# Kernel tuning notes

Hardware: AMD Instinct MI355X
Metric: run time of the kernel (lower is better)

The kernel has to match this reference:

```python
import jax, jax.numpy as jnp
import numpy as np

D_MODEL = 1024
BASE = 7
NUM_PLANES = 2
EPS = 1e-6


def setup_inputs() -> dict:
    key = jax.random.key(0)
    k_x, k_w, k_t, k_g = jax.random.split(key, 4)
    B, S, D = 4, 8192, D_MODEL
    x = jax.random.normal(k_x, (B, S, D), dtype=jnp.float32)
    # eidosTransform params: linear 3D -> D, then 2 planes of learned rotation angles over D/2 pairs
    W = jax.random.normal(k_w, (3 * D, D), dtype=jnp.float32) / np.sqrt(3 * D)
    b = jnp.zeros((D,), dtype=jnp.float32)
    theta = jax.random.normal(k_t, (NUM_PLANES, D // 2), dtype=jnp.float32) * 0.1
    # ModularPhaseNorm gain
    gamma = jnp.ones((D,), dtype=jnp.float32)
    return {"x": x, "W": W, "b": b, "theta": theta, "gamma": gamma}


def _eidos_transform(t, W, b, theta):
    # linear projection 3D -> D ('truncate' collapse to d_out)
    y = jnp.einsum("bse,ed->bsd", t, W) + b  # [B,S,D]
    B, S, D = y.shape
    # geometric mode: rotate (even, odd) dim pairs by learned angles, per plane
    for p in range(NUM_PLANES):
        yp = y.reshape(B, S, D // 2, 2)
        a, c2 = yp[..., 0], yp[..., 1]
        cos_t = jnp.cos(theta[p])
        sin_t = jnp.sin(theta[p])
        ra = a * cos_t - c2 * sin_t
        rb = a * sin_t + c2 * cos_t
        y = jnp.stack([ra, rb], axis=-1).reshape(B, S, D)
    return y


def _modular_phase_norm(y, gamma):
    # RMS-normalize within feature groups defined by (dim index mod BASE)
    D = y.shape[-1]
    group = jnp.arange(D) % BASE                      # [D]
    onehot = jax.nn.one_hot(group, BASE, dtype=y.dtype)  # [D, BASE]
    counts = onehot.sum(axis=0)                       # [BASE]
    ss = jnp.einsum("bsd,dg->bsg", y * y, onehot)     # [B,S,BASE]
    rms = jnp.sqrt(ss / counts + EPS)                 # [B,S,BASE]
    denom = rms[..., group]                           # [B,S,D]
    return y / denom * gamma


def reference(x, W, b, theta, gamma):
    B, S, D = x.shape
    zero_row = jnp.zeros((B, 1, D), dtype=x.dtype)
    left = jnp.concatenate([zero_row, x[:, :-1, :]], axis=1)   # roll +1, zero first
    right = jnp.concatenate([x[:, 1:, :], zero_row], axis=1)   # roll -1, zero last
    triplet = jnp.concatenate([left, x, right], axis=-1)        # [B,S,3D]
    mixed = _eidos_transform(triplet, W, b, theta)
    return _modular_phase_norm(mixed, gamma)
```

## Files before the change

### kernel.cpp

```cpp
#include <hip/hip_runtime.h>
#include <hip/hip_bf16.h>
#include <stdint.h>


#define SEQ 8192
#define NB 4
#define DM 1024
#define KD 3072

typedef __attribute__((ext_vector_type(8))) short short8_t;
typedef __attribute__((ext_vector_type(4))) float f32x4;

__device__ __forceinline__ unsigned short f2bf(float f) {
  union { float f; uint32_t u; } v; v.f = f;
  return (unsigned short)((v.u + 0x7fffu + ((v.u >> 16) & 1u)) >> 16);
}

__device__ __forceinline__ void async_ld16(const void* g, void* l) {
  __builtin_amdgcn_global_load_lds(
      (const __attribute__((address_space(1))) uint32_t*)g,
      (__attribute__((address_space(3))) uint32_t*)(uint32_t)(uintptr_t)l,
      16, 0, 0);
}

__global__ __launch_bounds__(256) void prep_w(const float* __restrict__ W,
                                              const float* __restrict__ theta,
                                              unsigned short* __restrict__ Wt) {
  __shared__ float csc[32], css[32];
  __shared__ unsigned short tile[64][72];
  const int bk = blockIdx.x % 48, bn = blockIdx.x / 48;
  const int k0 = bk * 64, n0 = bn * 64;
  const int t = threadIdx.x;
  if (t < 32) {
    int d = n0 / 2 + t;
    float ang = theta[d] + theta[512 + d];
    csc[t] = cosf(ang); css[t] = sinf(ang);
  }
  __syncthreads();
#pragma unroll
  for (int i = 0; i < 8; ++i) {
    int idx = i * 256 + t;
    int pr = idx >> 5;
    int pc = idx & 31;
    const float2 w2 = *(const float2*)&W[(size_t)(k0 + pr) * DM + n0 + pc * 2];
    float c = csc[pc], s = css[pc];
    tile[pc * 2][pr]     = f2bf(w2.x * c - w2.y * s);
    tile[pc * 2 + 1][pr] = f2bf(w2.x * s + w2.y * c);
  }
  __syncthreads();
#pragma unroll
  for (int i = 0; i < 16; ++i) {
    int idx = i * 256 + t;
    int r = idx >> 6, cdx = idx & 63;
    Wt[(size_t)(n0 + r) * KD + k0 + cdx] = tile[r][cdx];
  }
}

__global__ void prep_bias(const float* __restrict__ b, const float* __restrict__ theta,
                          float* __restrict__ biasp, float* __restrict__ zp) {
  const int t = threadIdx.x;
  float ang = theta[t] + theta[512 + t];
  float c = cosf(ang), s = sinf(ang);
  float be = b[2 * t], bo = b[2 * t + 1];
  biasp[2 * t]     = be * c - bo * s;
  biasp[2 * t + 1] = be * s + bo * c;
  if (t < 256) ((float4*)zp)[t] = make_float4(0.f, 0.f, 0.f, 0.f);
}

__global__ __launch_bounds__(256) void prep_x(const float* __restrict__ x,
                                              unsigned short* __restrict__ xbp) {
  const size_t total = (size_t)NB * 8194 * 128;
  for (size_t i = (size_t)blockIdx.x * 256 + threadIdx.x; i < total;
       i += (size_t)gridDim.x * 256) {
    int d8 = (int)(i & 127);
    size_t rem = i >> 7;
    int sp = (int)(rem % 8194);
    size_t bb = rem / 8194;
    uint4 o = make_uint4(0u, 0u, 0u, 0u);
    if (sp > 0 && sp < 8193) {
      const float4* src = (const float4*)(x + (bb * SEQ + (size_t)(sp - 1)) * DM + d8 * 8);
      float4 lo = src[0], hi = src[1];
      o.x = (uint32_t)f2bf(lo.x) | ((uint32_t)f2bf(lo.y) << 16);
      o.y = (uint32_t)f2bf(lo.z) | ((uint32_t)f2bf(lo.w) << 16);
      o.z = (uint32_t)f2bf(hi.x) | ((uint32_t)f2bf(hi.y) << 16);
      o.w = (uint32_t)f2bf(hi.z) | ((uint32_t)f2bf(hi.w) << 16);
    }
    ((uint4*)xbp)[i] = o;
  }
}

__global__ __launch_bounds__(512, 2) void gemm256(const unsigned short* __restrict__ xbp,
                                                  const unsigned short* __restrict__ Wt,
                                                  const float* __restrict__ biasp,
                                                  float* __restrict__ out) {
  __shared__ __align__(16) unsigned char As[4][16384];
  __shared__ __align__(16) unsigned char Bs[4][16384];

  const int tid = threadIdx.x;
  const int lane = tid & 63;
  const int wid = tid >> 6;
  const int wm = wid >> 2, wn = wid & 3;
  const int row16 = lane & 15, kgrp = lane >> 4;

  const int L = blockIdx.x;
  const int xcd = L & 7;
  const int j = L >> 3;
  const int mtile = xcd * 16 + (j >> 2);
  const int ntile = j & 3;

  const int n0 = ntile * 256;
  const int batch = mtile >> 5;
  const int s0 = (mtile & 31) * 256;
  const size_t m0 = (size_t)mtile * 256;

  auto stageA = [&](int kt, int buf) {
    const int c = kt >> 5;
    const int ksb = (kt & 31) * 32;
    const size_t base = ((size_t)batch * 8194 + (size_t)(s0 + c)) * DM + ksb;
#pragma unroll
    for (int i = 0; i < 2; ++i) {
      int idx = i * 512 + tid;
      int row = idx >> 2, c16 = idx & 3;
      int cs = c16 ^ ((row >> 1) & 3);
      async_ld16(xbp + base + (size_t)row * DM + cs * 8, &As[buf][idx * 16]);
    }
  };
  auto stageB = [&](int kt, int buf) {
    const int kb = kt * 32;
#pragma unroll
    for (int i = 0; i < 2; ++i) {
      int idx = i * 512 + tid;
      int row = idx >> 2, c16 = idx & 3;
      int cs = c16 ^ ((row >> 1) & 3);
      async_ld16(Wt + (size_t)(n0 + row) * KD + kb + cs * 8, &Bs[buf][idx * 16]);
    }
  };

  f32x4 acc[8][4];
#pragma unroll
  for (int a = 0; a < 8; ++a)
#pragma unroll
    for (int b = 0; b < 4; ++b) acc[a][b] = (f32x4){0.f, 0.f, 0.f, 0.f};

  stageA(0, 0); stageB(0, 0);
  stageA(1, 1); stageB(1, 1);
  stageA(2, 2); stageB(2, 2);
  asm volatile("s_waitcnt vmcnt(8)" ::: "memory");
  __builtin_amdgcn_s_barrier();

  for (int kt = 0; kt < 96; ++kt) {
    const int buf = kt & 3, sbuf = (kt + 3) & 3;
    const unsigned char* Ab = As[buf];
    const unsigned char* Bb = Bs[buf];
    short8_t af[4], bf[4];

#pragma unroll
    for (int mi = 0; mi < 4; ++mi) {
      int r = wm * 128 + mi * 16 + row16;
      af[mi] = *(const short8_t*)(Ab + r * 64 + (kgrp ^ ((r >> 1) & 3)) * 16);
    }
#pragma unroll
    for (int ni = 0; ni < 4; ++ni) {
      int r = wn * 64 + ni * 16 + row16;
      bf[ni] = *(const short8_t*)(Bb + r * 64 + (kgrp ^ ((r >> 1) & 3)) * 16);
    }
    if (kt < 93) stageA(kt + 3, sbuf);
    __builtin_amdgcn_s_barrier();
    asm volatile("s_waitcnt lgkmcnt(0)" ::: "memory");
    __builtin_amdgcn_sched_barrier(0);
    __builtin_amdgcn_s_setprio(1);
#pragma unroll
    for (int mi = 0; mi < 4; ++mi)
#pragma unroll
      for (int ni = 0; ni < 4; ++ni)
        acc[mi][ni] = __builtin_amdgcn_mfma_f32_16x16x32_bf16(
            af[mi], bf[ni], acc[mi][ni], 0, 0, 0);
    __builtin_amdgcn_s_setprio(0);
    __builtin_amdgcn_s_barrier();

#pragma unroll
    for (int mi = 0; mi < 4; ++mi) {
      int r = wm * 128 + 64 + mi * 16 + row16;
      af[mi] = *(const short8_t*)(Ab + r * 64 + (kgrp ^ ((r >> 1) & 3)) * 16);
    }
    if (kt < 93) stageB(kt + 3, sbuf);
    __builtin_amdgcn_s_barrier();
    asm volatile("s_waitcnt lgkmcnt(0)" ::: "memory");
    __builtin_amdgcn_sched_barrier(0);
    __builtin_amdgcn_s_setprio(1);
#pragma unroll
    for (int mi = 0; mi < 4; ++mi)
#pragma unroll
      for (int ni = 0; ni < 4; ++ni)
        acc[mi + 4][ni] = __builtin_amdgcn_mfma_f32_16x16x32_bf16(
            af[mi], bf[ni], acc[mi + 4][ni], 0, 0, 0);
    __builtin_amdgcn_s_setprio(0);
    if (kt < 93)      asm volatile("s_waitcnt vmcnt(8)" ::: "memory");
    else if (kt == 93) asm volatile("s_waitcnt vmcnt(4)" ::: "memory");
    else if (kt == 94) asm volatile("s_waitcnt vmcnt(0)" ::: "memory");
    __builtin_amdgcn_s_barrier();
  }

#pragma unroll
  for (int mi = 0; mi < 8; ++mi) {
    size_t grow = m0 + (size_t)(wm * 128 + mi * 16 + kgrp * 4);
#pragma unroll
    for (int ni = 0; ni < 4; ++ni) {
      int col = n0 + wn * 64 + ni * 16 + row16;
      float bia = biasp[col];
      float* op = out + grow * DM + col;
#pragma unroll
      for (int r = 0; r < 4; ++r) op[(size_t)r * DM] = acc[mi][ni][r] + bia;
    }
  }
}

__global__ __launch_bounds__(256) void gemm_fb(const float* __restrict__ Ag,
                                               const unsigned short* __restrict__ Wt,
                                               const float* __restrict__ biasp,
                                               const float* __restrict__ zp,
                                               float* __restrict__ out) {
  __shared__ __align__(16) unsigned char As[128 * 64 * 4];
  __shared__ __align__(16) unsigned char Bs[128 * 64 * 2];

  const int tid = threadIdx.x;
  const int lane = tid & 63;
  const int wid = tid >> 6;
  const int wm = wid >> 1, wn = wid & 1;
  const int row16 = lane & 15, kgrp = lane >> 4;

  const int L = blockIdx.x;
  const int xcd = L & 7;
  const int j = L >> 3;
  const int mtile = xcd * 32 + (j >> 3);
  const int ntile = j & 7;

  const int n0 = ntile * 128;
  const int batch = mtile >> 6;
  const int s0 = (mtile & 63) * 128;
  const size_t m0 = (size_t)mtile * 128;

  f32x4 acc[4][4];
#pragma unroll
  for (int a = 0; a < 4; ++a)
#pragma unroll
    for (int b = 0; b < 4; ++b) acc[a][b] = (f32x4){0.f, 0.f, 0.f, 0.f};

  for (int kt = 0; kt < 48; ++kt) {
    const int c = kt >> 4;
    const int ksb = (kt & 15) * 64;
    __syncthreads();
#pragma unroll
    for (int it = 0; it < 8; ++it) {
      int f16 = it * 256 + tid;
      int row = f16 >> 4, c16 = f16 & 15;
      int c16s = c16 ^ (row & 7);
      int s = s0 + row + c - 1;
      const float* src = (s >= 0 && s < SEQ)
          ? Ag + ((size_t)batch * SEQ + (size_t)s) * DM + ksb + c16s * 4
          : zp + c16s * 4;
      async_ld16(src, As + f16 * 16);
    }
#pragma unroll
    for (int it = 0; it < 4; ++it) {
      int f16 = it * 256 + tid;
      int row = f16 >> 3, c16 = f16 & 7;
      int c16s = c16 ^ (row & 7);
      const unsigned short* src = Wt + (size_t)(n0 + row) * KD + kt * 64 + c16s * 8;
      async_ld16(src, Bs + f16 * 16);
    }
    __syncthreads();

#pragma unroll
    for (int kk = 0; kk < 2; ++kk) {
      short8_t af[4], bfr[4];
#pragma unroll
      for (int mi = 0; mi < 4; ++mi) {
        int r = wm * 64 + mi * 16 + row16;
        int kb = kk * 128 + kgrp * 32;
        f32x4 lo = *(const f32x4*)(As + r * 256 + (kb ^ ((r & 7) << 4)));
        f32x4 hi = *(const f32x4*)(As + r * 256 + ((kb + 16) ^ ((r & 7) << 4)));
        union { short8_t v; unsigned short u[8]; } pk;
        pk.u[0] = f2bf(lo[0]); pk.u[1] = f2bf(lo[1]);
        pk.u[2] = f2bf(lo[2]); pk.u[3] = f2bf(lo[3]);
        pk.u[4] = f2bf(hi[0]); pk.u[5] = f2bf(hi[1]);
        pk.u[6] = f2bf(hi[2]); pk.u[7] = f2bf(hi[3]);
        af[mi] = pk.v;
      }
#pragma unroll
      for (int ni = 0; ni < 4; ++ni) {
        int r = wn * 64 + ni * 16 + row16;
        int kb = kk * 64 + kgrp * 16;
        bfr[ni] = *(const short8_t*)(Bs + r * 128 + (kb ^ ((r & 7) << 4)));
      }
#pragma unroll
      for (int mi = 0; mi < 4; ++mi)
#pragma unroll
        for (int ni = 0; ni < 4; ++ni)
          acc[mi][ni] = __builtin_amdgcn_mfma_f32_16x16x32_bf16(
              af[mi], bfr[ni], acc[mi][ni], 0, 0, 0);
    }
  }

#pragma unroll
  for (int mi = 0; mi < 4; ++mi) {
    size_t grow = m0 + (size_t)(wm * 64 + mi * 16 + kgrp * 4);
#pragma unroll
    for (int ni = 0; ni < 4; ++ni) {
      int col = n0 + wn * 64 + ni * 16 + row16;
      float bia = biasp[col];
      float* op = out + grow * DM + col;
#pragma unroll
      for (int r = 0; r < 4; ++r) op[(size_t)r * DM] = acc[mi][ni][r] + bia;
    }
  }
}

__global__ __launch_bounds__(256) void norm_kernel(float* __restrict__ y,
                                                   const float* __restrict__ gamma) {
  const int tid = threadIdx.x, lane = tid & 63, wv = tid >> 6;
  const size_t row = (size_t)blockIdx.x * 4 + wv;
  float4* rp = (float4*)(y + row * DM);
  const float4* gp = (const float4*)gamma;
  float4 v[4];
#pragma unroll
  for (int jj = 0; jj < 4; ++jj) v[jj] = rp[jj * 64 + lane];

  float ss[7] = {0.f, 0.f, 0.f, 0.f, 0.f, 0.f, 0.f};
#pragma unroll
  for (int jj = 0; jj < 4; ++jj) {
    const float vv[4] = {v[jj].x, v[jj].y, v[jj].z, v[jj].w};
#pragma unroll
    for (int i = 0; i < 4; ++i) {
      int d = (jj * 64 + lane) * 4 + i;
      int g = d % 7;
      float sq = vv[i] * vv[i];
#pragma unroll
      for (int t = 0; t < 7; ++t) ss[t] += (g == t) ? sq : 0.f;
    }
  }
#pragma unroll
  for (int t = 0; t < 7; ++t) {
#pragma unroll
    for (int off = 32; off >= 1; off >>= 1) ss[t] += __shfl_xor(ss[t], off, 64);
  }
  float inv[7];
#pragma unroll
  for (int t = 0; t < 7; ++t) {
    float cnt = (t < 2) ? 147.f : 146.f;
    inv[t] = rsqrtf(ss[t] / cnt + 1e-6f);
  }
#pragma unroll
  for (int jj = 0; jj < 4; ++jj) {
    float4 g4 = gp[jj * 64 + lane];
    const float vv[4] = {v[jj].x, v[jj].y, v[jj].z, v[jj].w};
    const float gg[4] = {g4.x, g4.y, g4.z, g4.w};
    float o[4];
#pragma unroll
    for (int i = 0; i < 4; ++i) {
      int d = (jj * 64 + lane) * 4 + i;
      int g = d % 7;
      float iv = inv[0];
#pragma unroll
      for (int t = 1; t < 7; ++t) iv = (g == t) ? inv[t] : iv;
      o[i] = vv[i] * iv * gg[i];
    }
    rp[jj * 64 + lane] = make_float4(o[0], o[1], o[2], o[3]);
  }
}

extern "C" void kernel_launch(void* const* d_in, const int* in_sizes, int n_in,
                              void* d_out, int out_size, void* d_ws, size_t ws_size,
                              hipStream_t stream) {
  const float* x     = (const float*)d_in[0];
  const float* W     = (const float*)d_in[1];
  const float* b     = (const float*)d_in[2];
  const float* theta = (const float*)d_in[3];
  const float* gamma = (const float*)d_in[4];
  float* out = (float*)d_out;
  (void)in_sizes; (void)n_in; (void)out_size;

  char* ws = (char*)d_ws;
  unsigned short* Wt = (unsigned short*)ws;
  float* biasp = (float*)(ws + 6291456);
  float* zp    = (float*)(ws + 6291456 + 4096);
  unsigned short* xbp = (unsigned short*)(ws + 6299648);
  const size_t needA = 6299648 + (size_t)NB * 8194 * DM * 2;

  prep_w<<<dim3(768), dim3(256), 0, stream>>>(W, theta, Wt);
  prep_bias<<<dim3(1), dim3(512), 0, stream>>>(b, theta, biasp, zp);

  if (ws_size >= needA) {
    prep_x<<<dim3(4096), dim3(256), 0, stream>>>(x, xbp);
    gemm256<<<dim3(512), dim3(512), 0, stream>>>(xbp, Wt, biasp, out);
  } else {
    gemm_fb<<<dim3(2048), dim3(256), 0, stream>>>(x, Wt, biasp, zp, out);
  }
  norm_kernel<<<dim3(8192), dim3(256), 0, stream>>>(out, gamma);
}
```

Measured before the change: 272.9 us.

## Prefetch next-tile LDS fragments into registers and cut barriers per k-step

Restructures the GEMM main loop so the fragments for the next k-tile are read from LDS into double-buffered registers while the current tile's MFMAs run, and both A and B global-to-LDS stages are issued together at the top of each step. Per-step barriers drop from four to one, and per-thread LDS offsets are precomputed once. The aim is to hide LDS read latency behind MFMA work and to reduce synchronisation stalls. In exchange, register pressure rises from the extra fragment buffers, and the waitcnt accounting becomes more delicate, with a risk of correctness issues if it is wrong.

```diff
diff --git a/kernel.cpp b/kernel.cpp
--- a/kernel.cpp
+++ b/kernel.cpp
@@ -113,6 +113,20 @@
   const int s0 = (mtile & 31) * 256;
   const size_t m0 = (size_t)mtile * 256;
 
+  int aoff[8], boff[4];
+#pragma unroll
+  for (int mi = 0; mi < 4; ++mi) {
+    int r = wm * 128 + mi * 16 + row16;
+    aoff[mi] = r * 64 + (kgrp ^ ((r >> 1) & 3)) * 16;
+    int r2 = r + 64;
+    aoff[mi + 4] = r2 * 64 + (kgrp ^ ((r2 >> 1) & 3)) * 16;
+  }
+#pragma unroll
+  for (int ni = 0; ni < 4; ++ni) {
+    int r = wn * 64 + ni * 16 + row16;
+    boff[ni] = r * 64 + (kgrp ^ ((r >> 1) & 3)) * 16;
+  }
+
   auto stageA = [&](int kt, int buf) {
     const int c = kt >> 5;
     const int ksb = (kt & 31) * 32;
@@ -142,31 +156,36 @@
 #pragma unroll
     for (int b = 0; b < 4; ++b) acc[a][b] = (f32x4){0.f, 0.f, 0.f, 0.f};
 
+  short8_t afA[4], bfA[4], afB[4], bfB[4], af1[4];
+
   stageA(0, 0); stageB(0, 0);
   stageA(1, 1); stageB(1, 1);
   stageA(2, 2); stageB(2, 2);
-  asm volatile("s_waitcnt vmcnt(8)" ::: "memory");
+  asm volatile("s_waitcnt vmcnt(4)" ::: "memory");
   __builtin_amdgcn_s_barrier();
-
-  for (int kt = 0; kt < 96; ++kt) {
-    const int buf = kt & 3, sbuf = (kt + 3) & 3;
-    const unsigned char* Ab = As[buf];
-    const unsigned char* Bb = Bs[buf];
-    short8_t af[4], bf[4];
-
-#pragma unroll
-    for (int mi = 0; mi < 4; ++mi) {
-      int r = wm * 128 + mi * 16 + row16;
-      af[mi] = *(const short8_t*)(Ab + r * 64 + (kgrp ^ ((r >> 1) & 3)) * 16);
-    }
-#pragma unroll
-    for (int ni = 0; ni < 4; ++ni) {
-      int r = wn * 64 + ni * 16 + row16;
-      bf[ni] = *(const short8_t*)(Bb + r * 64 + (kgrp ^ ((r >> 1) & 3)) * 16);
-    }
-    if (kt < 93) stageA(kt + 3, sbuf);
-    __builtin_amdgcn_s_barrier();
-    asm volatile("s_waitcnt lgkmcnt(0)" ::: "memory");
+#pragma unroll
+  for (int mi = 0; mi < 4; ++mi) afA[mi] = *(const short8_t*)(&As[0][0] + aoff[mi]);
+#pragma unroll
+  for (int ni = 0; ni < 4; ++ni) bfA[ni] = *(const short8_t*)(&Bs[0][0] + boff[ni]);
+  asm volatile("s_waitcnt lgkmcnt(0)" ::: "memory");
+  __builtin_amdgcn_sched_barrier(0);
+
+  auto body = [&](int kt, int buf, int doStage, int doNext, int vm4,
+                  short8_t (&afC)[4], short8_t (&bfC)[4],
+                  short8_t (&afN)[4], short8_t (&bfN)[4]) {
+    const int nbuf = (buf + 1) & 3, sbuf = (buf + 3) & 3;
+    if (doStage) { stageA(kt + 3, sbuf); stageB(kt + 3, sbuf); }
+#pragma unroll
+    for (int mi = 0; mi < 4; ++mi)
+      af1[mi] = *(const short8_t*)(&As[buf][0] + aoff[mi + 4]);
+    if (doNext) {
+#pragma unroll
+      for (int mi = 0; mi < 4; ++mi)
+        afN[mi] = *(const short8_t*)(&As[nbuf][0] + aoff[mi]);
+#pragma unroll
+      for (int ni = 0; ni < 4; ++ni)
+        bfN[ni] = *(const short8_t*)(&Bs[nbuf][0] + boff[ni]);
+    }
     __builtin_amdgcn_sched_barrier(0);
     __builtin_amdgcn_s_setprio(1);
 #pragma unroll
@@ -174,18 +193,10 @@
 #pragma unroll
       for (int ni = 0; ni < 4; ++ni)
         acc[mi][ni] = __builtin_amdgcn_mfma_f32_16x16x32_bf16(
-            af[mi], bf[ni], acc[mi][ni], 0, 0, 0);
+            afC[mi], bfC[ni], acc[mi][ni], 0, 0, 0);
     __builtin_amdgcn_s_setprio(0);
-    __builtin_amdgcn_s_barrier();
-
-#pragma unroll
-    for (int mi = 0; mi < 4; ++mi) {
-      int r = wm * 128 + 64 + mi * 16 + row16;
-      af[mi] = *(const short8_t*)(Ab + r * 64 + (kgrp ^ ((r >> 1) & 3)) * 16);
-    }
-    if (kt < 93) stageB(kt + 3, sbuf);
-    __builtin_amdgcn_s_barrier();
-    asm volatile("s_waitcnt lgkmcnt(0)" ::: "memory");
+    if (doNext) asm volatile("s_waitcnt lgkmcnt(8)" ::: "memory");
+    else        asm volatile("s_waitcnt lgkmcnt(0)" ::: "memory");
     __builtin_amdgcn_sched_barrier(0);
     __builtin_amdgcn_s_setprio(1);
 #pragma unroll
@@ -193,13 +204,24 @@
 #pragma unroll
       for (int ni = 0; ni < 4; ++ni)
         acc[mi + 4][ni] = __builtin_amdgcn_mfma_f32_16x16x32_bf16(
-            af[mi], bf[ni], acc[mi + 4][ni], 0, 0, 0);
+            af1[mi], bfC[ni], acc[mi + 4][ni], 0, 0, 0);
     __builtin_amdgcn_s_setprio(0);
-    if (kt < 93)      asm volatile("s_waitcnt vmcnt(8)" ::: "memory");
-    else if (kt == 93) asm volatile("s_waitcnt vmcnt(4)" ::: "memory");
-    else if (kt == 94) asm volatile("s_waitcnt vmcnt(0)" ::: "memory");
+    if (vm4) asm volatile("s_waitcnt vmcnt(4) lgkmcnt(0)" ::: "memory");
+    else     asm volatile("s_waitcnt vmcnt(0) lgkmcnt(0)" ::: "memory");
+    __builtin_amdgcn_sched_barrier(0);
     __builtin_amdgcn_s_barrier();
-  }
+  };
+
+  for (int kt4 = 0; kt4 < 92; kt4 += 4) {
+    body(kt4 + 0, 0, 1, 1, 1, afA, bfA, afB, bfB);
+    body(kt4 + 1, 1, 1, 1, 1, afB, bfB, afA, bfA);
+    body(kt4 + 2, 2, 1, 1, 1, afA, bfA, afB, bfB);
+    body(kt4 + 3, 3, 1, 1, 1, afB, bfB, afA, bfA);
+  }
+  body(92, 0, 1, 1, 1, afA, bfA, afB, bfB);
+  body(93, 1, 0, 1, 0, afB, bfB, afA, bfA);
+  body(94, 2, 0, 1, 0, afA, bfA, afB, bfB);
+  body(95, 3, 0, 0, 0, afB, bfB, afA, bfA);
 
 #pragma unroll
   for (int mi = 0; mi < 8; ++mi) {
```

New measurement: 262.0 us. 4.0% less time.

## Split GEMM block into 16 waves of 64x64 tiles with one barrier per k-step

Applied to the files above, without the earlier changes.

The 256x256 GEMM block now launches 1024 threads instead of 512, so each of its 16 waves owns a 64x64 sub-tile and holds half the accumulators. The k-loop is reorganised to issue both A and B async stages at the top of each step, with one barrier per step instead of several. The loop is unrolled by four so LDS buffer indices are constants, and LDS read offsets are computed once up front. The intent is more waves per CU to hide latency and less synchronisation, at the cost of lower MFMA reuse per wave and more LDS reads. The launch bound of (1024, 4) may also squeeze the per-thread register budget.

```diff
diff --git a/kernel.cpp b/kernel.cpp
--- a/kernel.cpp
+++ b/kernel.cpp
@@ -89,10 +89,10 @@
   }
 }
 
-__global__ __launch_bounds__(512, 2) void gemm256(const unsigned short* __restrict__ xbp,
-                                                  const unsigned short* __restrict__ Wt,
-                                                  const float* __restrict__ biasp,
-                                                  float* __restrict__ out) {
+__global__ __launch_bounds__(1024, 4) void gemm256(const unsigned short* __restrict__ xbp,
+                                                   const unsigned short* __restrict__ Wt,
+                                                   const float* __restrict__ biasp,
+                                                   float* __restrict__ out) {
   __shared__ __align__(16) unsigned char As[4][16384];
   __shared__ __align__(16) unsigned char Bs[4][16384];
 
@@ -113,59 +113,53 @@
   const int s0 = (mtile & 31) * 256;
   const size_t m0 = (size_t)mtile * 256;
 
+  int aoff[4], boff[4];
+#pragma unroll
+  for (int mi = 0; mi < 4; ++mi) {
+    int r = wm * 64 + mi * 16 + row16;
+    aoff[mi] = r * 64 + (kgrp ^ ((r >> 1) & 3)) * 16;
+  }
+#pragma unroll
+  for (int ni = 0; ni < 4; ++ni) {
+    int r = wn * 64 + ni * 16 + row16;
+    boff[ni] = r * 64 + (kgrp ^ ((r >> 1) & 3)) * 16;
+  }
+
+  const int srow = tid >> 2, sc16 = tid & 3;
+  const int scs = sc16 ^ ((srow >> 1) & 3);
   auto stageA = [&](int kt, int buf) {
     const int c = kt >> 5;
     const int ksb = (kt & 31) * 32;
     const size_t base = ((size_t)batch * 8194 + (size_t)(s0 + c)) * DM + ksb;
-#pragma unroll
-    for (int i = 0; i < 2; ++i) {
-      int idx = i * 512 + tid;
-      int row = idx >> 2, c16 = idx & 3;
-      int cs = c16 ^ ((row >> 1) & 3);
-      async_ld16(xbp + base + (size_t)row * DM + cs * 8, &As[buf][idx * 16]);
-    }
+    async_ld16(xbp + base + (size_t)srow * DM + scs * 8, &As[buf][tid * 16]);
   };
   auto stageB = [&](int kt, int buf) {
     const int kb = kt * 32;
-#pragma unroll
-    for (int i = 0; i < 2; ++i) {
-      int idx = i * 512 + tid;
-      int row = idx >> 2, c16 = idx & 3;
-      int cs = c16 ^ ((row >> 1) & 3);
-      async_ld16(Wt + (size_t)(n0 + row) * KD + kb + cs * 8, &Bs[buf][idx * 16]);
-    }
+    async_ld16(Wt + (size_t)(n0 + srow) * KD + kb + scs * 8, &Bs[buf][tid * 16]);
   };
 
-  f32x4 acc[8][4];
-#pragma unroll
-  for (int a = 0; a < 8; ++a)
+  f32x4 acc[4][4];
+#pragma unroll
+  for (int a = 0; a < 4; ++a)
 #pragma unroll
     for (int b = 0; b < 4; ++b) acc[a][b] = (f32x4){0.f, 0.f, 0.f, 0.f};
 
   stageA(0, 0); stageB(0, 0);
   stageA(1, 1); stageB(1, 1);
   stageA(2, 2); stageB(2, 2);
-  asm volatile("s_waitcnt vmcnt(8)" ::: "memory");
+  asm volatile("s_waitcnt vmcnt(4)" ::: "memory");
   __builtin_amdgcn_s_barrier();
 
-  for (int kt = 0; kt < 96; ++kt) {
-    const int buf = kt & 3, sbuf = (kt + 3) & 3;
-    const unsigned char* Ab = As[buf];
-    const unsigned char* Bb = Bs[buf];
+  auto body = [&](int kt, int buf, int doStage, int vmN) {
+    const int sbuf = (buf + 3) & 3;
+    if (doStage) { stageA(kt + 3, sbuf); stageB(kt + 3, sbuf); }
     short8_t af[4], bf[4];
-
-#pragma unroll
-    for (int mi = 0; mi < 4; ++mi) {
-      int r = wm * 128 + mi * 16 + row16;
-      af[mi] = *(const short8_t*)(Ab + r * 64 + (kgrp ^ ((r >> 1) & 3)) * 16);
-    }
-#pragma unroll
-    for (int ni = 0; ni < 4; ++ni) {
-      int r = wn * 64 + ni * 16 + row16;
-      bf[ni] = *(const short8_t*)(Bb + r * 64 + (kgrp ^ ((r >> 1) & 3)) * 16);
-    }
-    if (kt < 93) stageA(kt + 3, sbuf);
-    __builtin_amdgcn_s_barrier();
+#pragma unroll
+    for (int mi = 0; mi < 4; ++mi)
+      af[mi] = *(const short8_t*)(&As[buf][0] + aoff[mi]);
+#pragma unroll
+    for (int ni = 0; ni < 4; ++ni)
+      bf[ni] = *(const short8_t*)(&Bs[buf][0] + boff[ni]);
     asm volatile("s_waitcnt lgkmcnt(0)" ::: "memory");
     __builtin_amdgcn_sched_barrier(0);
     __builtin_amdgcn_s_setprio(1);
@@ -176,34 +170,27 @@
         acc[mi][ni] = __builtin_amdgcn_mfma_f32_16x16x32_bf16(
             af[mi], bf[ni], acc[mi][ni], 0, 0, 0);
     __builtin_amdgcn_s_setprio(0);
+    if (vmN == 4)      asm volatile("s_waitcnt vmcnt(4)" ::: "memory");
+    else if (vmN == 2) asm volatile("s_waitcnt vmcnt(2)" ::: "memory");
+    else               asm volatile("s_waitcnt vmcnt(0)" ::: "memory");
+    __builtin_amdgcn_sched_barrier(0);
     __builtin_amdgcn_s_barrier();
-
-#pragma unroll
-    for (int mi = 0; mi < 4; ++mi) {
-      int r = wm * 128 + 64 + mi * 16 + row16;
-      af[mi] = *(const short8_t*)(Ab + r * 64 + (kgrp ^ ((r >> 1) & 3)) * 16);
-    }
-    if (kt < 93) stageB(kt + 3, sbuf);
-    __builtin_amdgcn_s_barrier();
-    asm volatile("s_waitcnt lgkmcnt(0)" ::: "memory");
-    __builtin_amdgcn_sched_barrier(0);
-    __builtin_amdgcn_s_setprio(1);
-#pragma unroll
-    for (int mi = 0; mi < 4; ++mi)
-#pragma unroll
-      for (int ni = 0; ni < 4; ++ni)
-        acc[mi + 4][ni] = __builtin_amdgcn_mfma_f32_16x16x32_bf16(
-            af[mi], bf[ni], acc[mi + 4][ni], 0, 0, 0);
-    __builtin_amdgcn_s_setprio(0);
-    if (kt < 93)      asm volatile("s_waitcnt vmcnt(8)" ::: "memory");
-    else if (kt == 93) asm volatile("s_waitcnt vmcnt(4)" ::: "memory");
-    else if (kt == 94) asm volatile("s_waitcnt vmcnt(0)" ::: "memory");
-    __builtin_amdgcn_s_barrier();
-  }
-
-#pragma unroll
-  for (int mi = 0; mi < 8; ++mi) {
-    size_t grow = m0 + (size_t)(wm * 128 + mi * 16 + kgrp * 4);
+  };
+
+  for (int kt4 = 0; kt4 < 92; kt4 += 4) {
+    body(kt4 + 0, 0, 1, 4);
+    body(kt4 + 1, 1, 1, 4);
+    body(kt4 + 2, 2, 1, 4);
+    body(kt4 + 3, 3, 1, 4);
+  }
+  body(92, 0, 1, 4);
+  body(93, 1, 0, 2);
+  body(94, 2, 0, 0);
+  body(95, 3, 0, 0);
+
+#pragma unroll
+  for (int mi = 0; mi < 4; ++mi) {
+    size_t grow = m0 + (size_t)(wm * 64 + mi * 16 + kgrp * 4);
 #pragma unroll
     for (int ni = 0; ni < 4; ++ni) {
       int col = n0 + wn * 64 + ni * 16 + row16;
@@ -392,7 +379,7 @@
 
   if (ws_size >= needA) {
     prep_x<<<dim3(4096), dim3(256), 0, stream>>>(x, xbp);
-    gemm256<<<dim3(512), dim3(512), 0, stream>>>(xbp, Wt, biasp, out);
+    gemm256<<<dim3(512), dim3(1024), 0, stream>>>(xbp, Wt, biasp, out);
   } else {
     gemm_fb<<<dim3(2048), dim3(256), 0, stream>>>(x, Wt, biasp, zp, out);
   }
```

Measured after the change: 257.3 us. -5.7%, faster.
